# Performance work log

Measured on AMD Instinct MI355X. Metric: run time of the kernel, lower is better.

## Reference

```python
import jax, jax.numpy as jnp
import numpy as np

N = 262144  # points
C = 256     # backbone_out_channels
K = 20      # semantic_num_classes
BN_EPS = 1e-3
EPS = 1e-8
IGNORE = -1


def setup_inputs() -> dict:
    key = jax.random.key(0)
    ks = jax.random.split(key, 12)
    feat = jax.random.normal(ks[0], (N, C), dtype=jnp.float32)
    coord = jax.random.normal(ks[1], (N, 3), dtype=jnp.float32)
    instance_centroid = jax.random.normal(ks[2], (N, 3), dtype=jnp.float32)
    segment = jax.random.randint(ks[3], (N,), 0, K, dtype=jnp.int32)
    instance = jax.random.randint(ks[4], (N,), 0, 1000, dtype=jnp.int32)
    # bias_head: Linear(C,C) -> BN1d(C) -> ReLU -> Linear(C,3)
    w1 = jax.random.normal(ks[5], (C, C), dtype=jnp.float32) * 0.02
    b1 = jnp.zeros((C,), dtype=jnp.float32)
    gamma = jnp.ones((C,), dtype=jnp.float32)
    beta = jnp.zeros((C,), dtype=jnp.float32)
    w2 = jax.random.normal(ks[6], (C, 3), dtype=jnp.float32) * 0.02
    b2 = jnp.zeros((3,), dtype=jnp.float32)
    # seg_head: Linear(C, K)
    ws = jax.random.normal(ks[7], (C, K), dtype=jnp.float32) * 0.02
    bs = jnp.zeros((K,), dtype=jnp.float32)
    return dict(feat=feat, coord=coord, instance_centroid=instance_centroid,
                segment=segment, instance=instance,
                w1=w1, b1=b1, gamma=gamma, beta=beta, w2=w2, b2=b2, ws=ws, bs=bs)


def reference(feat, coord, instance_centroid, segment, instance,
              w1, b1, gamma, beta, w2, b2, ws, bs):
    # bias head: Linear -> BatchNorm1d (training stats) -> ReLU -> Linear
    h = feat @ w1 + b1                                  # [N, C]
    mu = jnp.mean(h, axis=0)
    var = jnp.mean((h - mu) ** 2, axis=0)               # biased var (torch BN)
    h = (h - mu) * jax.lax.rsqrt(var + BN_EPS) * gamma + beta
    h = jax.nn.relu(h)
    bias_pred = h @ w2 + b2                             # [N, 3]

    logit_pred = feat @ ws + bs                         # [N, K]

    # semantic cross-entropy with ignore_index
    valid = segment != IGNORE
    tgt = jnp.where(valid, segment, 0)
    logp = jax.nn.log_softmax(logit_pred, axis=-1)
    nll = -jnp.take_along_axis(logp, tgt[:, None], axis=1)[:, 0]
    vf = valid.astype(logit_pred.dtype)
    seg_loss = jnp.sum(nll * vf) / (jnp.sum(vf) + EPS)

    # masked bias L1 loss
    mask = (instance != IGNORE).astype(bias_pred.dtype)
    bias_gt = instance_centroid - coord                 # [N, 3]
    bias_dist = jnp.sum(jnp.abs(bias_pred - bias_gt), axis=-1)
    msum = jnp.sum(mask) + EPS
    bias_l1_loss = jnp.sum(bias_dist * mask) / msum

    # masked cosine (direction) loss
    pred_n = bias_pred / (jnp.linalg.norm(bias_pred, axis=1, keepdims=True) + EPS)
    gt_n = bias_gt / (jnp.linalg.norm(bias_gt, axis=1, keepdims=True) + EPS)
    cos = -jnp.sum(pred_n * gt_n, axis=-1)
    bias_cosine_loss = jnp.sum(cos * mask) / msum

    loss = seg_loss + bias_l1_loss + bias_cosine_loss
    return jnp.stack([loss, seg_loss, bias_l1_loss, bias_cosine_loss])
```

## Files before the change

### kernel.cpp

```cpp
#include <hip/hip_runtime.h>
#include <cstdio>
#include <cstdint>

typedef unsigned int u32;
typedef unsigned short u16;
typedef short bf16x8 __attribute__((ext_vector_type(8)));
typedef float f32x4 __attribute__((ext_vector_type(4)));

#define NPTS 262144
#define CDIM 256
#define KCLS 20
#define NBLK 4096
#define NSLOT 256
#define LSLOT 256

#define OFF_WT    ((size_t)134217728)
#define OFF_W2T   (OFF_WT + (size_t)163840)
#define OFF_AGGBN (OFF_W2T + (size_t)8192)
#define OFF_AGGNL (OFF_AGGBN + (size_t)524288)
#define OFF_AGGL  (OFF_AGGNL + (size_t)2048)
#define OFF_AB    (OFF_AGGL + (size_t)4096)
#define WS_NEED   (OFF_AB + (size_t)2048)
#define MEMSET_OFF OFF_AGGBN
#define MEMSET_LEN ((size_t)(524288 + 2048 + 4096))

__device__ __forceinline__ u16 bf16rne(float x) {
    u32 u = __float_as_uint(x);
    u32 r = u + 0x7FFFu + ((u >> 16) & 1u);
    return (u16)(r >> 16);
}
__device__ __forceinline__ float bf2f(u16 b) {
    return __uint_as_float(((u32)b) << 16);
}

__global__ void k_prep(const float* __restrict__ w1, const float* __restrict__ wsm,
                       const float* __restrict__ w2,
                       u16* __restrict__ Wt2, u16* __restrict__ w2t) {
    int k = blockIdx.x;
    int n = threadIdx.x;
    float v = 0.f;
    if (n < 256) v = w1[k * 256 + n];
    else if (n < 256 + KCLS) v = wsm[k * KCLS + (n - 256)];
    Wt2[((size_t)(k >> 3) * 320 + n) * 8 + (k & 7)] = bf16rne(v);
    if (n < 16) w2t[n * 256 + k] = bf16rne((n < 3) ? w2[k * 3 + n] : 0.f);
}

__global__ __launch_bounds__(256, 3) void k_gemm(
    const float* __restrict__ feat, const float* __restrict__ b1,
    const float* __restrict__ bs, const int* __restrict__ segment,
    const u16* __restrict__ Wt2, u16* __restrict__ h_out,
    float* __restrict__ aggBN, float* __restrict__ aggNLL)
{
    __shared__ uint4 smem4[2560];
    uint4* const As4 = smem4;
    uint4* const Bs4 = smem4 + 512;

    const int t = threadIdx.x;
    const int lane = t & 63;
    const int wv = t >> 6;
    const int q = lane >> 4;
    const int i16 = lane & 15;
    const int row0 = blockIdx.x * 64;
    const int slot = blockIdx.x & (NSLOT - 1);

    const f32x4 fz = {0.f, 0.f, 0.f, 0.f};
    f32x4 acc[4][4];
    f32x4 lacc[2];
#pragma unroll
    for (int r = 0; r < 4; ++r)
#pragma unroll
        for (int c = 0; c < 4; ++c) acc[r][c] = fz;
    lacc[0] = fz; lacc[1] = fz;

    const int sm = t >> 2;
    const int sq = t & 3;
    const float* fsrc = feat + (size_t)(row0 + sm) * 256 + sq * 8;
    const int wsl = sm ^ (sq << 2);
    const int As_slot0 = sq * 64 + wsl;
    const int As_slot1 = (sq + 4) * 64 + wsl;

    float4 f0 = *(const float4*)(fsrc);
    float4 f1 = *(const float4*)(fsrc + 4);
    float4 f2 = *(const float4*)(fsrc + 32);
    float4 f3 = *(const float4*)(fsrc + 36);

#pragma unroll 1
    for (int kc = 0; kc < 4; ++kc) {
        {
            uint4 pk;
            pk.x = (u32)bf16rne(f0.x) | ((u32)bf16rne(f0.y) << 16);
            pk.y = (u32)bf16rne(f0.z) | ((u32)bf16rne(f0.w) << 16);
            pk.z = (u32)bf16rne(f1.x) | ((u32)bf16rne(f1.y) << 16);
            pk.w = (u32)bf16rne(f1.z) | ((u32)bf16rne(f1.w) << 16);
            As4[As_slot0] = pk;
            pk.x = (u32)bf16rne(f2.x) | ((u32)bf16rne(f2.y) << 16);
            pk.y = (u32)bf16rne(f2.z) | ((u32)bf16rne(f2.w) << 16);
            pk.z = (u32)bf16rne(f3.x) | ((u32)bf16rne(f3.y) << 16);
            pk.w = (u32)bf16rne(f3.z) | ((u32)bf16rne(f3.w) << 16);
            As4[As_slot1] = pk;
        }
#pragma unroll
        for (int i = 0; i < 4; ++i) {
            const u16* src0 = Wt2 + ((size_t)(kc * 8 + wv) * 320 + i * 64 + lane) * 8;
            u32* dst0 = (u32*)&Bs4[wv * 256 + i * 64];
            __builtin_amdgcn_global_load_lds(
                (const __attribute__((address_space(1))) u32*)src0,
                (__attribute__((address_space(3))) u32*)dst0, 16, 0, 0);
            const u16* src1 = Wt2 + ((size_t)(kc * 8 + wv + 4) * 320 + i * 64 + lane) * 8;
            u32* dst1 = (u32*)&Bs4[(wv + 4) * 256 + i * 64];
            __builtin_amdgcn_global_load_lds(
                (const __attribute__((address_space(1))) u32*)(src1),
                (__attribute__((address_space(3))) u32*)dst1, 16, 0, 0);
        }
        __syncthreads();

        float4 fn0, fn1, fn2, fn3;
        if (kc < 3) {
            const float* p = fsrc + (kc + 1) * 64;
            fn0 = *(const float4*)(p);
            fn1 = *(const float4*)(p + 4);
            fn2 = *(const float4*)(p + 32);
            fn3 = *(const float4*)(p + 36);
        }

#pragma unroll
        for (int s = 0; s < 2; ++s) {
            const int kq = s * 4 + q;
            bf16x8 lbf[2];
#pragma unroll
            for (int x = 0; x < 2; ++x)
                lbf[x] = *(const bf16x8*)(Wt2 +
                    ((size_t)(kc * 8 + kq) * 320 + 256 + x * 16 + i16) * 8);
            bf16x8 bfr[4], af[4], la;
#pragma unroll
            for (int c = 0; c < 4; ++c)
                bfr[c] = *(const bf16x8*)&Bs4[kq * 256 + wv * 64 + c * 16 + i16];
#pragma unroll
            for (int r = 0; r < 4; ++r)
                af[r] = *(const bf16x8*)&As4[kq * 64 + ((r * 16 + i16) ^ (q << 2))];
            la = *(const bf16x8*)&As4[kq * 64 + ((wv * 16 + i16) ^ (q << 2))];

#pragma unroll
            for (int r = 0; r < 4; ++r)
#pragma unroll
                for (int c = 0; c < 4; ++c)
                    acc[r][c] = __builtin_amdgcn_mfma_f32_16x16x32_bf16(af[r], bfr[c], acc[r][c], 0, 0, 0);
#pragma unroll
            for (int x = 0; x < 2; ++x)
                lacc[x] = __builtin_amdgcn_mfma_f32_16x16x32_bf16(la, lbf[x], lacc[x], 0, 0, 0);
        }
        __syncthreads();
        f0 = fn0; f1 = fn1; f2 = fn2; f3 = fn3;
    }

    float b1v[4];
#pragma unroll
    for (int c = 0; c < 4; ++c) b1v[c] = b1[wv * 64 + c * 16 + i16];
    float bsv0 = bs[i16];
    float bsv1 = (16 + i16 < KCLS) ? bs[16 + i16] : 0.f;

    float nllacc = 0.f, cntacc = 0.f;
#pragma unroll
    for (int j = 0; j < 4; ++j) {
        int rowr = row0 + wv * 16 + q * 4 + j;
        float l0 = lacc[0][j] + bsv0;
        float l1raw = lacc[1][j] + bsv1;
        float l1m = (i16 < 4) ? l1raw : -3.0e38f;
        float mx = fmaxf(l0, l1m);
#pragma unroll
        for (int d = 1; d < 16; d <<= 1) mx = fmaxf(mx, __shfl_xor(mx, d));
        float s = __expf(l0 - mx) + ((i16 < 4) ? __expf(l1raw - mx) : 0.f);
#pragma unroll
        for (int d = 1; d < 16; d <<= 1) s += __shfl_xor(s, d);
        int tg = segment[rowr];
        float v0 = __shfl(l0, (lane & 48) + (tg & 15));
        float v1 = __shfl(l1raw, (lane & 48) + ((tg - 16) & 15));
        float lt = (tg < 16) ? v0 : v1;
        if (i16 == 0 && tg >= 0) {
            nllacc += __logf(s) + mx - lt;
            cntacc += 1.f;
        }
    }
#pragma unroll
    for (int d = 1; d < 64; d <<= 1) {
        nllacc += __shfl_xor(nllacc, d);
        cntacc += __shfl_xor(cntacc, d);
    }
    if (lane == 0) {
        atomicAdd(aggNLL + slot * 2 + 0, nllacc);
        atomicAdd(aggNLL + slot * 2 + 1, cntacc);
    }

#pragma unroll
    for (int c = 0; c < 4; ++c) {
        float s1 = 0.f, s2 = 0.f;
#pragma unroll
        for (int r = 0; r < 4; ++r)
#pragma unroll
            for (int j = 0; j < 4; ++j) {
                float v = acc[r][c][j] + b1v[c];
                s1 += v; s2 = fmaf(v, v, s2);
            }
        s1 += __shfl_xor(s1, 16); s1 += __shfl_xor(s1, 32);
        s2 += __shfl_xor(s2, 16); s2 += __shfl_xor(s2, 32);
        if (q == 0) {
            int ch = wv * 64 + c * 16 + i16;
            atomicAdd(aggBN + slot * 512 + ch, s1);
            atomicAdd(aggBN + slot * 512 + 256 + ch, s2);
        }
    }

    u16* Ht = (u16*)smem4;
#pragma unroll
    for (int r = 0; r < 4; ++r)
#pragma unroll
        for (int c = 0; c < 4; ++c)
#pragma unroll
            for (int j = 0; j < 4; ++j) {
                float v = acc[r][c][j] + b1v[c];
                int rw = r * 16 + q * 4 + j;
                int cl = wv * 64 + c * 16 + i16;
                Ht[rw * 264 + cl] = bf16rne(v);
            }
    __syncthreads();
#pragma unroll
    for (int i = 0; i < 8; ++i) {
        int c2 = i * 256 + t;
        int rb = c2 >> 9;
        int kc = (c2 >> 6) & 7;
        int qq = (c2 >> 4) & 3;
        int r16 = c2 & 15;
        uint4 v = *(const uint4*)((const char*)smem4 + (rb * 16 + r16) * 528 + kc * 64 + qq * 16);
        *(uint4*)((char*)h_out + (size_t)(blockIdx.x * 4 + rb) * 8192 + (size_t)(c2 & 511) * 16) = v;
    }
}

__global__ void k_reduce(const float* __restrict__ gamma, const float* __restrict__ beta,
                         const float* __restrict__ aggBN,
                         float* __restrict__ Aarr, float* __restrict__ Barr) {
    int c = blockIdx.x;
    int l = threadIdx.x;
    float s1 = 0.f, s2 = 0.f;
#pragma unroll
    for (int i = 0; i < 4; ++i) {
        int s = l + i * 64;
        s1 += aggBN[s * 512 + c];
        s2 += aggBN[s * 512 + 256 + c];
    }
#pragma unroll
    for (int d = 1; d < 64; d <<= 1) {
        s1 += __shfl_xor(s1, d);
        s2 += __shfl_xor(s2, d);
    }
    if (l == 0) {
        const float inv = 1.f / (float)NPTS;
        float mu = s1 * inv;
        float var = fmaxf(s2 * inv - mu * mu, 0.f);
        float a = gamma[c] * rsqrtf(var + 1e-3f);
        Aarr[c] = a;
        Barr[c] = beta[c] - mu * a;
    }
}

__global__ __launch_bounds__(256) void k_loss(
    const u16* __restrict__ h, const float* __restrict__ Aarr, const float* __restrict__ Barr,
    const u16* __restrict__ w2t, const float* __restrict__ b2,
    const float* __restrict__ coord, const float* __restrict__ cent,
    const int* __restrict__ inst, float* __restrict__ aggL)
{
    __shared__ float bp[4][16][4];
    __shared__ float red[12];

    const int t = threadIdx.x;
    const int lane = t & 63;
    const int wv = t >> 6;
    const int q = lane >> 4;
    const int i16 = lane & 15;
    const int row0 = blockIdx.x * 64;
    const int rb = blockIdx.x * 4 + wv;

    const u16* hb = h + (size_t)rb * 4096 + q * 128 + i16 * 8;
    bf16x8 hf[8];
#pragma unroll
    for (int kc = 0; kc < 8; ++kc)
        hf[kc] = *(const bf16x8*)(hb + kc * 512);

    bf16x8 wfr[8];
#pragma unroll
    for (int kc = 0; kc < 8; ++kc)
        wfr[kc] = *(const bf16x8*)(w2t + (size_t)i16 * 256 + kc * 32 + q * 8);
    float b2x = b2[0], b2y = b2[1], b2z = b2[2];

    const f32x4 fz = {0.f, 0.f, 0.f, 0.f};
    f32x4 c = fz;
#pragma unroll
    for (int kc = 0; kc < 8; ++kc) {
        float4 a0 = *(const float4*)(Aarr + kc * 32 + q * 8);
        float4 a1 = *(const float4*)(Aarr + kc * 32 + q * 8 + 4);
        float4 b0 = *(const float4*)(Barr + kc * 32 + q * 8);
        float4 b1 = *(const float4*)(Barr + kc * 32 + q * 8 + 4);
        float av[8] = {a0.x, a0.y, a0.z, a0.w, a1.x, a1.y, a1.z, a1.w};
        float bv[8] = {b0.x, b0.y, b0.z, b0.w, b1.x, b1.y, b1.z, b1.w};
        bf16x8 hn;
#pragma unroll
        for (int j = 0; j < 8; ++j) {
            float x = fmaxf(fmaf(bf2f(((const u16*)&hf[kc])[j]), av[j], bv[j]), 0.f);
            ((u16*)&hn)[j] = bf16rne(x);
        }
        c = __builtin_amdgcn_mfma_f32_16x16x32_bf16(hn, wfr[kc], c, 0, 0, 0);
    }

    if (i16 < 3) {
#pragma unroll
        for (int j = 0; j < 4; ++j) bp[wv][q * 4 + j][i16] = c[j];
    }
    float l1a = 0.f, cosa = 0.f, ma = 0.f;
    if (lane < 16) {
        int row = row0 + wv * 16 + lane;
        float4 P = *(const float4*)bp[wv][lane];
        float bpx = P.x + b2x, bpy = P.y + b2y, bpz = P.z + b2z;
        const float* cp = coord + (size_t)row * 3;
        const float* ip = cent + (size_t)row * 3;
        float gx = ip[0] - cp[0], gy = ip[1] - cp[1], gz = ip[2] - cp[2];
        float mk = (inst[row] != -1) ? 1.f : 0.f;
        float l1 = fabsf(bpx - gx) + fabsf(bpy - gy) + fabsf(bpz - gz);
        float np = sqrtf(fmaf(bpx, bpx, fmaf(bpy, bpy, bpz * bpz)));
        float ng = sqrtf(fmaf(gx, gx, fmaf(gy, gy, gz * gz)));
        float dp = fmaf(bpx, gx, fmaf(bpy, gy, bpz * gz));
        float cosv = -dp / ((np + 1e-8f) * (ng + 1e-8f));
        l1a = l1 * mk;
        cosa = cosv * mk;
        ma = mk;
    }
#pragma unroll
    for (int d = 1; d < 64; d <<= 1) {
        l1a += __shfl_xor(l1a, d);
        cosa += __shfl_xor(cosa, d);
        ma += __shfl_xor(ma, d);
    }
    if (lane == 0) { red[wv] = l1a; red[4 + wv] = cosa; red[8 + wv] = ma; }
    __syncthreads();
    if (t == 0) {
        int slot = blockIdx.x & (LSLOT - 1);
        atomicAdd(aggL + slot * 4 + 0, red[0] + red[1] + red[2] + red[3]);
        atomicAdd(aggL + slot * 4 + 1, red[4] + red[5] + red[6] + red[7]);
        atomicAdd(aggL + slot * 4 + 2, red[8] + red[9] + red[10] + red[11]);
    }
}

__global__ void k_final(const float* __restrict__ aggNLL, const float* __restrict__ aggL,
                        float* __restrict__ out) {
    int lane = threadIdx.x;
    float nll = 0.f, cnt = 0.f, l1 = 0.f, cs = 0.f, mk = 0.f;
#pragma unroll
    for (int i = 0; i < 4; ++i) {
        int s = lane + i * 64;
        nll += aggNLL[s * 2 + 0];
        cnt += aggNLL[s * 2 + 1];
        l1 += aggL[s * 4 + 0];
        cs += aggL[s * 4 + 1];
        mk += aggL[s * 4 + 2];
    }
#pragma unroll
    for (int d = 1; d < 64; d <<= 1) {
        nll += __shfl_xor(nll, d);
        cnt += __shfl_xor(cnt, d);
        l1 += __shfl_xor(l1, d);
        cs += __shfl_xor(cs, d);
        mk += __shfl_xor(mk, d);
    }
    if (lane == 0) {
        float seg = nll / (cnt + 1e-8f);
        float l1l = l1 / (mk + 1e-8f);
        float csl = cs / (mk + 1e-8f);
        out[0] = seg + l1l + csl;
        out[1] = seg;
        out[2] = l1l;
        out[3] = csl;
    }
}

extern "C" void kernel_launch(void* const* d_in, const int* in_sizes, int n_in,
                              void* d_out, int out_size, void* d_ws, size_t ws_size,
                              hipStream_t stream) {
    const float* feat   = (const float*)d_in[0];
    const float* coord  = (const float*)d_in[1];
    const float* cent   = (const float*)d_in[2];
    const int* segment  = (const int*)d_in[3];
    const int* inst     = (const int*)d_in[4];
    const float* w1     = (const float*)d_in[5];
    const float* b1     = (const float*)d_in[6];
    const float* gamma  = (const float*)d_in[7];
    const float* beta   = (const float*)d_in[8];
    const float* w2     = (const float*)d_in[9];
    const float* b2     = (const float*)d_in[10];
    const float* wsm    = (const float*)d_in[11];
    const float* bs     = (const float*)d_in[12];
    float* out = (float*)d_out;

    char* wsb = (char*)d_ws;
    u16* h_ws    = (u16*)wsb;
    u16* Wt2     = (u16*)(wsb + OFF_WT);
    u16* w2t     = (u16*)(wsb + OFF_W2T);
    float* aggBN = (float*)(wsb + OFF_AGGBN);
    float* aggNL = (float*)(wsb + OFF_AGGNL);
    float* aggL  = (float*)(wsb + OFF_AGGL);
    float* Aarr  = (float*)(wsb + OFF_AB);
    float* Barr  = Aarr + 256;

    if (ws_size < WS_NEED)
        fprintf(stderr, "kernel_launch: ws_size=%zu < needed %zu — WILL CORRUPT\n",
                ws_size, (size_t)WS_NEED);

    hipMemsetAsync(wsb + MEMSET_OFF, 0, MEMSET_LEN, stream);
    k_prep<<<256, 320, 0, stream>>>(w1, wsm, w2, Wt2, w2t);
    k_gemm<<<NBLK, 256, 0, stream>>>(feat, b1, bs, segment, Wt2, h_ws, aggBN, aggNL);
    k_reduce<<<256, 64, 0, stream>>>(gamma, beta, aggBN, Aarr, Barr);
    k_loss<<<4096, 256, 0, stream>>>(h_ws, Aarr, Barr, w2t, b2, coord, cent, inst, aggL);
    k_final<<<1, 64, 0, stream>>>(aggNL, aggL, out);
}
```

Measured before the change: 486.2 us.

## Double-buffer weight tiles in LDS and prefetch the next K-chunk during MFMA

```diff
diff --git a/kernel.cpp b/kernel.cpp
--- a/kernel.cpp
+++ b/kernel.cpp
@@ -45,15 +45,13 @@
     if (n < 16) w2t[n * 256 + k] = bf16rne((n < 3) ? w2[k * 3 + n] : 0.f);
 }
 
-__global__ __launch_bounds__(256, 3) void k_gemm(
+__global__ __launch_bounds__(256) void k_gemm(
     const float* __restrict__ feat, const float* __restrict__ b1,
     const float* __restrict__ bs, const int* __restrict__ segment,
     const u16* __restrict__ Wt2, u16* __restrict__ h_out,
     float* __restrict__ aggBN, float* __restrict__ aggNLL)
 {
-    __shared__ uint4 smem4[2560];
-    uint4* const As4 = smem4;
-    uint4* const Bs4 = smem4 + 512;
+    __shared__ uint4 smem4[5120];
 
     const int t = threadIdx.x;
     const int lane = t & 63;
@@ -79,6 +77,19 @@
     const int As_slot0 = sq * 64 + wsl;
     const int As_slot1 = (sq + 4) * 64 + wsl;
 
+#pragma unroll
+    for (int i = 0; i < 4; ++i) {
+        const u16* src0 = Wt2 + ((size_t)(wv) * 320 + i * 64 + lane) * 8;
+        __builtin_amdgcn_global_load_lds(
+            (const __attribute__((address_space(1))) u32*)src0,
+            (__attribute__((address_space(3))) u32*)&smem4[1024 + wv * 256 + i * 64],
+            16, 0, 0);
+        const u16* src1 = Wt2 + ((size_t)(wv + 4) * 320 + i * 64 + lane) * 8;
+        __builtin_amdgcn_global_load_lds(
+            (const __attribute__((address_space(1))) u32*)src1,
+            (__attribute__((address_space(3))) u32*)&smem4[1024 + (wv + 4) * 256 + i * 64],
+            16, 0, 0);
+    }
     float4 f0 = *(const float4*)(fsrc);
     float4 f1 = *(const float4*)(fsrc + 4);
     float4 f2 = *(const float4*)(fsrc + 32);
@@ -86,6 +97,10 @@
 
 #pragma unroll 1
     for (int kc = 0; kc < 4; ++kc) {
+        const int pb = kc & 1;
+        uint4* const As4 = smem4 + pb * 512;
+        uint4* const Bs4 = smem4 + 1024 + pb * 2048;
+
         {
             uint4 pk;
             pk.x = (u32)bf16rne(f0.x) | ((u32)bf16rne(f0.y) << 16);
@@ -99,23 +114,23 @@
             pk.w = (u32)bf16rne(f3.z) | ((u32)bf16rne(f3.w) << 16);
             As4[As_slot1] = pk;
         }
-#pragma unroll
-        for (int i = 0; i < 4; ++i) {
-            const u16* src0 = Wt2 + ((size_t)(kc * 8 + wv) * 320 + i * 64 + lane) * 8;
-            u32* dst0 = (u32*)&Bs4[wv * 256 + i * 64];
-            __builtin_amdgcn_global_load_lds(
-                (const __attribute__((address_space(1))) u32*)src0,
-                (__attribute__((address_space(3))) u32*)dst0, 16, 0, 0);
-            const u16* src1 = Wt2 + ((size_t)(kc * 8 + wv + 4) * 320 + i * 64 + lane) * 8;
-            u32* dst1 = (u32*)&Bs4[(wv + 4) * 256 + i * 64];
-            __builtin_amdgcn_global_load_lds(
-                (const __attribute__((address_space(1))) u32*)(src1),
-                (__attribute__((address_space(3))) u32*)dst1, 16, 0, 0);
-        }
-        __syncthreads();
 
         float4 fn0, fn1, fn2, fn3;
         if (kc < 3) {
+            uint4* const Bn4 = smem4 + 1024 + (pb ^ 1) * 2048;
+#pragma unroll
+            for (int i = 0; i < 4; ++i) {
+                const u16* src0 = Wt2 + ((size_t)((kc + 1) * 8 + wv) * 320 + i * 64 + lane) * 8;
+                __builtin_amdgcn_global_load_lds(
+                    (const __attribute__((address_space(1))) u32*)src0,
+                    (__attribute__((address_space(3))) u32*)&Bn4[wv * 256 + i * 64],
+                    16, 0, 0);
+                const u16* src1 = Wt2 + ((size_t)((kc + 1) * 8 + wv + 4) * 320 + i * 64 + lane) * 8;
+                __builtin_amdgcn_global_load_lds(
+                    (const __attribute__((address_space(1))) u32*)src1,
+                    (__attribute__((address_space(3))) u32*)&Bn4[(wv + 4) * 256 + i * 64],
+                    16, 0, 0);
+            }
             const float* p = fsrc + (kc + 1) * 64;
             fn0 = *(const float4*)(p);
             fn1 = *(const float4*)(p + 4);
@@ -123,6 +138,9 @@
             fn3 = *(const float4*)(p + 36);
         }
 
+        asm volatile("s_waitcnt lgkmcnt(0)" ::: "memory");
+        __builtin_amdgcn_s_barrier();
+
 #pragma unroll
         for (int s = 0; s < 2; ++s) {
             const int kq = s * 4 + q;
@@ -149,8 +167,11 @@
             for (int x = 0; x < 2; ++x)
                 lacc[x] = __builtin_amdgcn_mfma_f32_16x16x32_bf16(la, lbf[x], lacc[x], 0, 0, 0);
         }
-        __syncthreads();
-        f0 = fn0; f1 = fn1; f2 = fn2; f3 = fn3;
+
+        asm volatile("s_waitcnt lgkmcnt(0)" ::: "memory");
+        __builtin_amdgcn_s_barrier();
+
+        if (kc < 3) { f0 = fn0; f1 = fn1; f2 = fn2; f3 = fn3; }
     }
 
     float b1v[4];
```

New measurement: 488.9 us. No clear change (+0.6%).
